# Optimization experiments

Hardware: AMD Instinct MI355X
Metric: run time of the kernel (lower is better)

The kernel has to match this reference:

```python
import jax, jax.numpy as jnp
import numpy as np

G, N, F_IN, H, C = 128, 512, 128, 128, 10
LAMB = 1.0
NEG_SLOPE = 0.2
P_EDGE = 32.0 / N  # avg degree ~32


def setup_inputs() -> dict:
    key = jax.random.key(0)
    ks = jax.random.split(key, 12)
    x = jax.random.normal(ks[0], (G, N, F_IN), dtype=jnp.float32)
    # symmetric 0/1 adjacency without self loops (per-graph dense block)
    a = (jax.random.uniform(ks[1], (G, N, N)) < P_EDGE).astype(jnp.float32)
    adj = jnp.maximum(a, jnp.swapaxes(a, 1, 2)) * (1.0 - jnp.eye(N, dtype=jnp.float32))

    def lin(k, fi, fo):
        return (jax.random.normal(k, (fi, fo), dtype=jnp.float32) / np.float32(np.sqrt(fi)))

    return {
        "x": x, "adj": adj,
        "W1": lin(ks[2], F_IN, H), "b1": jnp.zeros((H,), jnp.float32),
        "W2": lin(ks[3], H, H), "b2": jnp.zeros((H,), jnp.float32),
        "W3": lin(ks[4], H, H), "b3": jnp.zeros((H,), jnp.float32),
        "att1_s": 0.1 * jax.random.normal(ks[5], (H,), dtype=jnp.float32),
        "att1_d": 0.1 * jax.random.normal(ks[6], (H,), dtype=jnp.float32),
        "att2_s": 0.1 * jax.random.normal(ks[7], (H,), dtype=jnp.float32),
        "att2_d": 0.1 * jax.random.normal(ks[8], (H,), dtype=jnp.float32),
        "Wl1": lin(ks[9], 2 * H, H), "bl1": jnp.zeros((H,), jnp.float32),
        "Wl2": lin(ks[10], H, H // 2), "bl2": jnp.zeros((H // 2,), jnp.float32),
        "Wl3": lin(ks[11], H // 2, C), "bl3": jnp.zeros((C,), jnp.float32),
    }


def gcn(x, adj, W, b):
    # GCNConv: D^{-1/2} (A + I) D^{-1/2} X W + b  (self-loop weight 1, edge weights in adj)
    deg = adj.sum(-1) + 1.0                              # [G, n]
    dinv = jax.lax.rsqrt(deg)
    xw = x @ W                                           # [G, n, H]
    agg = jnp.einsum('gij,gjf->gif', adj, dinv[..., None] * xw)
    return dinv[..., None] * agg + (dinv * dinv)[..., None] * xw + b


def info_score(x, adj):
    # HGP-SL node information score: row-wise L1 norm of (I - D^{-1} A) X
    deg = jnp.maximum(adj.sum(-1), 1.0)
    agg = jnp.einsum('gij,gjf->gif', adj, x) / deg[..., None]
    return jnp.sum(jnp.abs(x - agg), axis=-1)            # [G, n]


def hgpsl_pool(x, adj, att_s, att_d, k):
    # top-k node selection by information score, then structure learning:
    # dense (sample=False) path: e_ij = leaky_relu(att.[x_i||x_j]) + lamb*A_ij, softmax over j
    s = info_score(x, adj)
    _, idx = jax.lax.top_k(s, k)                         # [G, k]
    xk = jnp.take_along_axis(x, idx[..., None], axis=1)  # [G, k, H]
    g = jnp.arange(x.shape[0])[:, None, None]
    ak = adj[g, idx[:, :, None], idx[:, None, :]]        # induced adjacency [G, k, k]
    e = jax.nn.leaky_relu((xk @ att_s)[:, :, None] + (xk @ att_d)[:, None, :], NEG_SLOPE)
    attn = jax.nn.softmax(e + LAMB * ak, axis=-1)        # new learned edge weights
    return xk, attn


def readout(x):
    # gmp || gap over nodes
    return jnp.concatenate([x.max(axis=1), x.mean(axis=1)], axis=-1)


def reference(x, adj, W1, b1, W2, b2, W3, b3, att1_s, att1_d, att2_s, att2_d,
              Wl1, bl1, Wl2, bl2, Wl3, bl3):
    h = jax.nn.relu(gcn(x, adj, W1, b1))
    h, a1 = hgpsl_pool(h, adj, att1_s, att1_d, N // 2)
    x1 = readout(h)
    h = jax.nn.relu(gcn(h, a1, W2, b2))
    h, a2 = hgpsl_pool(h, a1, att2_s, att2_d, N // 4)
    x2 = readout(h)
    h = jax.nn.relu(gcn(h, a2, W3, b3))
    x3 = readout(h)
    z = jax.nn.relu(x1) + jax.nn.relu(x2) + jax.nn.relu(x3)
    z = jax.nn.relu(z @ Wl1 + bl1)
    z = jax.nn.relu(z @ Wl2 + bl2)
    return jax.nn.softmax(z @ Wl3 + bl3, axis=-1)
```

## Files before the change

### kernel.cpp

```cpp
#include <hip/hip_runtime.h>

#define Gg   128
#define N1   512
#define FH   128
#define K1   256
#define K2   128

typedef __bf16 bf16x8 __attribute__((ext_vector_type(8)));
typedef float  floatx4 __attribute__((ext_vector_type(4)));

__device__ inline float wredsum(float v) {
#pragma unroll
    for (int o = 32; o; o >>= 1) v += __shfl_xor(v, o, 64);
    return v;
}
__device__ inline float wredmax(float v) {
#pragma unroll
    for (int o = 32; o; o >>= 1) v = fmaxf(v, __shfl_xor(v, o, 64));
    return v;
}
__device__ inline unsigned short bf_rne(float x) {
    unsigned u = __float_as_uint(x);
    return (unsigned short)((u + 0x7fffu + ((u >> 16) & 1u)) >> 16);
}
__device__ __forceinline__ void gll16(const void* gsrc, void* lds) {
    __builtin_amdgcn_global_load_lds(
        (const __attribute__((address_space(1))) unsigned int*)gsrc,
        (__attribute__((address_space(3))) unsigned int*)lds, 16, 0, 0);
}

__global__ __launch_bounds__(256) void k_prep(const float* __restrict__ adj,
        unsigned short* __restrict__ adjbf,
        float* __restrict__ dinv_gcn, float* __restrict__ dinv_info) {
    int wave = threadIdx.x >> 6, lane = threadIdx.x & 63;
    long long row = (long long)blockIdx.x * 4 + wave;
    const float* ar = adj + row * N1;
    float s = 0.f;
    unsigned short ub[8] __attribute__((aligned(16)));
#pragma unroll
    for (int c = 0; c < 2; ++c) {
        float4 v = *(const float4*)(ar + lane * 8 + c * 4);
        s += (v.x + v.y) + (v.z + v.w);
        ub[c * 4 + 0] = (unsigned short)(__float_as_uint(v.x) >> 16);
        ub[c * 4 + 1] = (unsigned short)(__float_as_uint(v.y) >> 16);
        ub[c * 4 + 2] = (unsigned short)(__float_as_uint(v.z) >> 16);
        ub[c * 4 + 3] = (unsigned short)(__float_as_uint(v.w) >> 16);
    }
    *(uint4*)(adjbf + row * N1 + lane * 8) = *(const uint4*)ub;
    s = wredsum(s);
    if (lane == 0) {
        dinv_gcn[row]  = rsqrtf(s + 1.0f);
        dinv_info[row] = 1.0f / fmaxf(s, 1.0f);
    }
}

__global__ __launch_bounds__(256) void k_tsplit(const float* __restrict__ feat,
        unsigned short* __restrict__ Thi, unsigned short* __restrict__ Tmid,
        unsigned short* __restrict__ Tlo) {
    __shared__ float tile[64 * 65];
    int b = blockIdx.x;
    int g = b >> 4, rb = (b >> 1) & 7, cb = b & 1;
    int t = threadIdx.x;
    {
        int r0 = t >> 4, c4 = t & 15;
#pragma unroll
        for (int i = 0; i < 4; ++i) {
            int r = r0 + i * 16;
            float4 v = *(const float4*)(feat + ((long long)g * 512 + rb * 64 + r) * 128 + cb * 64 + c4 * 4);
            tile[r * 65 + c4 * 4 + 0] = v.x;
            tile[r * 65 + c4 * 4 + 1] = v.y;
            tile[r * 65 + c4 * 4 + 2] = v.z;
            tile[r * 65 + c4 * 4 + 3] = v.w;
        }
    }
    __syncthreads();
    int tf = t >> 2, chunk = t & 3;
    unsigned short hbuf[16] __attribute__((aligned(16)));
    unsigned short mbuf[16] __attribute__((aligned(16)));
    unsigned short lbuf[16] __attribute__((aligned(16)));
#pragma unroll
    for (int i = 0; i < 16; ++i) {
        int m = chunk * 16 + i;
        float v = tile[m * 65 + tf];
        unsigned short h = bf_rne(v);
        float fh = __uint_as_float((unsigned)h << 16);
        float r1 = v - fh;
        unsigned short md = bf_rne(r1);
        float fm = __uint_as_float((unsigned)md << 16);
        float r2 = r1 - fm;
        unsigned short lo = bf_rne(r2);
        hbuf[i] = h; mbuf[i] = md; lbuf[i] = lo;
    }
    int sxz = (tf >> 1) & 3;
    int c0 = (chunk & 1) * 2;
    int p0 = (c0 ^ sxz) * 8, p1 = ((c0 + 1) ^ sxz) * 8;
    long long obase = (long long)g * 65536 + (rb * 2 + (chunk >> 1)) * 4096
                    + (cb * 64 + tf) * 32;
    *(uint4*)(Thi + obase + p0)  = *(const uint4*)&hbuf[0];
    *(uint4*)(Thi + obase + p1)  = *(const uint4*)&hbuf[8];
    *(uint4*)(Tmid + obase + p0) = *(const uint4*)&mbuf[0];
    *(uint4*)(Tmid + obase + p1) = *(const uint4*)&mbuf[8];
    *(uint4*)(Tlo + obase + p0)  = *(const uint4*)&lbuf[0];
    *(uint4*)(Tlo + obase + p1)  = *(const uint4*)&lbuf[8];
}

template<int EPI>
__global__ __launch_bounds__(256) void k_aggmm(const unsigned short* __restrict__ adjbf,
        const unsigned short* __restrict__ Bhi, const unsigned short* __restrict__ Bmid,
        const unsigned short* __restrict__ Blo,
        const float* __restrict__ dvec, const float* __restrict__ hx,
        const float* __restrict__ bias, float* __restrict__ outH, float* __restrict__ outS) {
    __shared__ unsigned short Al[4096];
    __shared__ unsigned short Blin[3][4096];
    __shared__ float sred[2][128];
    int b = blockIdx.x;
    int g  = (b & 7) + ((b >> 5) << 3);
    int rb = (b >> 3) & 3;
    int tid = threadIdx.x;
    int w = tid >> 6, lane = tid & 63;
    int wm = w >> 1, wn = w & 1;
    int ln = lane & 15, quad = lane >> 4;
    int aoff = ((quad ^ ((lane >> 1) & 3)) << 4);
    floatx4 acc[4][4];
#pragma unroll
    for (int i = 0; i < 4; ++i)
#pragma unroll
        for (int j = 0; j < 4; ++j) { floatx4 z = {0.f, 0.f, 0.f, 0.f}; acc[i][j] = z; }

    const char* bsrc0 = (const char*)(Bhi  + (long long)g * 65536);
    const char* bsrc1 = (const char*)(Bmid + (long long)g * 65536);
    const char* bsrc2 = (const char*)(Blo  + (long long)g * 65536);
    int r1 = w * 32 + (lane >> 2);
    int c1 = (lane & 3) ^ ((r1 >> 1) & 3);
    int r2 = r1 + 16;
    int c2 = (lane & 3) ^ ((r2 >> 1) & 3);
    const unsigned short* abase = adjbf + ((long long)g * 512 + rb * 128) * 512;
    const unsigned short* asrc1 = abase + (long long)r1 * 512 + c1 * 8;
    const unsigned short* asrc2 = abase + (long long)r2 * 512 + c2 * 8;
    char* aldst = (char*)Al + w * 2048;

    for (int kk = 0; kk < 512; kk += 32) {
        __syncthreads();
        gll16(asrc1 + kk, aldst);
        gll16(asrc2 + kk, aldst + 1024);
        {
            long long soff = (long long)(kk >> 5) * 8192 + (w * 2048) + (lane << 4);
            char* l0 = (char*)&Blin[0][0] + w * 2048;
            char* l1 = (char*)&Blin[1][0] + w * 2048;
            char* l2 = (char*)&Blin[2][0] + w * 2048;
            gll16(bsrc0 + soff,        l0);
            gll16(bsrc0 + soff + 1024, l0 + 1024);
            gll16(bsrc1 + soff,        l1);
            gll16(bsrc1 + soff + 1024, l1 + 1024);
            gll16(bsrc2 + soff,        l2);
            gll16(bsrc2 + soff + 1024, l2 + 1024);
        }
        __syncthreads();
        bf16x8 af[4];
#pragma unroll
        for (int tm = 0; tm < 4; ++tm)
            af[tm] = *(const bf16x8*)((const char*)Al + (wm * 64 + tm * 16 + ln) * 64 + aoff);
#pragma unroll
        for (int s = 0; s < 3; ++s) {
#pragma unroll
            for (int tn = 0; tn < 4; ++tn) {
                bf16x8 bfr = *(const bf16x8*)((const char*)&Blin[s][0]
                                              + (wn * 64 + tn * 16 + ln) * 64 + aoff);
#pragma unroll
                for (int tm = 0; tm < 4; ++tm)
                    acc[tm][tn] = __builtin_amdgcn_mfma_f32_16x16x32_bf16(af[tm], bfr, acc[tm][tn], 0, 0, 0);
            }
        }
    }
    long long rowbase = (long long)g * 512 + rb * 128;
    if (EPI == 0) {
#pragma unroll
        for (int tm = 0; tm < 4; ++tm)
#pragma unroll
        for (int r = 0; r < 4; ++r) {
            int ml = wm * 64 + tm * 16 + quad * 4 + r;
            long long grow = rowbase + ml;
            float di = dvec[grow];
#pragma unroll
            for (int tn = 0; tn < 4; ++tn) {
                int nc = wn * 64 + tn * 16 + ln;
                float hv = hx[grow * 128 + nc];
                float o = fmaxf(fmaf(di, acc[tm][tn][r] + hv, bias[nc]), 0.f);
                outH[grow * 128 + nc] = o;
            }
        }
    } else {
#pragma unroll
        for (int tm = 0; tm < 4; ++tm)
#pragma unroll
        for (int r = 0; r < 4; ++r) {
            int ml = wm * 64 + tm * 16 + quad * 4 + r;
            long long grow = rowbase + ml;
            float di = dvec[grow];
            float v = 0.f;
#pragma unroll
            for (int tn = 0; tn < 4; ++tn) {
                int nc = wn * 64 + tn * 16 + ln;
                float hv = hx[grow * 128 + nc];
                v += fabsf(hv - acc[tm][tn][r] * di);
            }
            v += __shfl_xor(v, 1); v += __shfl_xor(v, 2);
            v += __shfl_xor(v, 4); v += __shfl_xor(v, 8);
            if (ln == 0) sred[wn][ml] = v;
        }
        __syncthreads();
        if (tid < 128) outS[rowbase + tid] = sred[0][tid] + sred[1][tid];
    }
}

__global__ __launch_bounds__(256) void k_gemm_rw(const float* __restrict__ A,
        const float* __restrict__ W, float* __restrict__ C,
        const float* __restrict__ rs) {
    __shared__ float Al[64][68];
    __shared__ float Wl[64][132];
    long long row0 = (long long)blockIdx.x * 64;
    int tid = threadIdx.x, tr = tid >> 4, tc = tid & 15;
    float acc[4][8] = {};
    for (int ch = 0; ch < 2; ++ch) {
        for (int p = tid; p < 1024; p += 256) {
            int r = p >> 4, c4 = p & 15;
            *(float4*)&Al[r][c4 * 4] = *(const float4*)(A + (row0 + r) * 128 + ch * 64 + c4 * 4);
        }
        for (int p = tid; p < 2048; p += 256) {
            int r = p >> 5, c4 = p & 31;
            *(float4*)&Wl[r][c4 * 4] = *(const float4*)(W + (ch * 64 + r) * 128 + c4 * 4);
        }
        __syncthreads();
        for (int k = 0; k < 64; ++k) {
            float4 w0 = *(const float4*)&Wl[k][tc * 8];
            float4 w1 = *(const float4*)&Wl[k][tc * 8 + 4];
            float w[8] = {w0.x, w0.y, w0.z, w0.w, w1.x, w1.y, w1.z, w1.w};
#pragma unroll
            for (int i = 0; i < 4; ++i) {
                float a = Al[tr * 4 + i][k];
#pragma unroll
                for (int j = 0; j < 8; ++j) acc[i][j] = fmaf(a, w[j], acc[i][j]);
            }
        }
        __syncthreads();
    }
#pragma unroll
    for (int i = 0; i < 4; ++i) {
        long long r = row0 + tr * 4 + i;
        float sc = rs ? rs[r] : 1.0f;
        *(float4*)(C + r * 128 + tc * 8)     = make_float4(sc * acc[i][0], sc * acc[i][1], sc * acc[i][2], sc * acc[i][3]);
        *(float4*)(C + r * 128 + tc * 8 + 4) = make_float4(sc * acc[i][4], sc * acc[i][5], sc * acc[i][6], sc * acc[i][7]);
    }
}

template<int NT, int KSEL>
__global__ __launch_bounds__(256) void k_topk(const float* __restrict__ s, int* __restrict__ idx) {
    __shared__ unsigned long long keys[NT];
    int g = blockIdx.x;
    const float* sg = s + g * NT;
    for (int t = threadIdx.x; t < NT; t += 256) {
        unsigned int b = __float_as_uint(sg[t]);
        unsigned int ord = (b & 0x80000000u) ? ~b : (b | 0x80000000u);
        keys[t] = ((unsigned long long)(~ord) << 32) | (unsigned int)t;
    }
    __syncthreads();
    for (int k = 2; k <= NT; k <<= 1) {
        for (int j = k >> 1; j > 0; j >>= 1) {
            for (int i = threadIdx.x; i < NT; i += 256) {
                int l = i ^ j;
                if (l > i) {
                    bool dir = ((i & k) == 0);
                    unsigned long long a = keys[i], b2 = keys[l];
                    bool sw = dir ? (a > b2) : (a < b2);
                    if (sw) { keys[i] = b2; keys[l] = a; }
                }
            }
            __syncthreads();
        }
    }
    for (int t = threadIdx.x; t < KSEL; t += 256)
        idx[g * KSEL + t] = (int)(keys[t] & 0xffffffffu);
}

template<int KK>
__global__ __launch_bounds__(256) void k_gather(const float* __restrict__ h, int srcN,
        const int* __restrict__ idx, const float* __restrict__ atts, const float* __restrict__ attd,
        float* __restrict__ xk, float* __restrict__ as_, float* __restrict__ ad_) {
    int wave = threadIdx.x >> 6, lane = threadIdx.x & 63;
    int r = blockIdx.x * 4 + wave;
    int g = r / KK;
    int j = idx[r];
    float2 v = *(const float2*)(h + ((long long)g * srcN + j) * 128 + lane * 2);
    *(float2*)(xk + (long long)r * 128 + lane * 2) = v;
    float2 sv = *(const float2*)(atts + lane * 2);
    float2 dv = *(const float2*)(attd + lane * 2);
    float ps = v.x * sv.x + v.y * sv.y;
    float pd = v.x * dv.x + v.y * dv.y;
    ps = wredsum(ps); pd = wredsum(pd);
    if (lane == 0) { as_[r] = ps; ad_[r] = pd; }
}

template<int KK, int SRCN>
__global__ __launch_bounds__(256) void k_attn(const float* __restrict__ adjSrc,
        const int* __restrict__ idx, const float* __restrict__ as_, const float* __restrict__ ad_,
        float* __restrict__ attn, float* __restrict__ dgo, float* __restrict__ dio) {
    constexpr int E = KK / 64;
    __shared__ int   idxL[KK];
    __shared__ float adL[KK];
    __shared__ float rowL[4][SRCN];
    int bpg = KK / 4;
    int g = blockIdx.x / bpg;
    int wave = threadIdx.x >> 6, lane = threadIdx.x & 63;
    int i = (blockIdx.x % bpg) * 4 + wave;
    for (int t = threadIdx.x; t < KK; t += 256) { idxL[t] = idx[g * KK + t]; adL[t] = ad_[g * KK + t]; }
    __syncthreads();
    int ri = idxL[i];
    const float* arow = adjSrc + ((long long)g * SRCN + ri) * SRCN;
    for (int c = lane; c < SRCN; c += 64) rowL[wave][c] = arow[c];
    float asi = as_[g * KK + i];
    float vals[E];
    float m = -1e30f;
#pragma unroll
    for (int e = 0; e < E; ++e) {
        int j = e * 64 + lane;
        float x = asi + adL[j];
        x = (x >= 0.f) ? x : 0.2f * x;
        x += rowL[wave][idxL[j]];
        vals[e] = x; m = fmaxf(m, x);
    }
    m = wredmax(m);
    float S = 0.f;
#pragma unroll
    for (int e = 0; e < E; ++e) { vals[e] = expf(vals[e] - m); S += vals[e]; }
    S = wredsum(S);
    float inv = 1.f / S, rs = 0.f;
    float* orow = attn + ((long long)g * KK + i) * KK;
#pragma unroll
    for (int e = 0; e < E; ++e) { float p = vals[e] * inv; rs += p; orow[e * 64 + lane] = p; }
    rs = wredsum(rs);
    if (lane == 0) { dgo[g * KK + i] = rsqrtf(rs + 1.f); dio[g * KK + i] = 1.f / fmaxf(rs, 1.f); }
}

template<int KK>
__global__ __launch_bounds__(128) void k_readout(const float* __restrict__ xk, float* __restrict__ xo) {
    int g = blockIdx.x, f = threadIdx.x;
    const float* p = xk + (long long)g * KK * 128 + f;
    float m = -1e30f, s = 0.f;
    for (int r = 0; r < KK; ++r) { float v = p[r * 128]; m = fmaxf(m, v); s += v; }
    xo[g * 256 + f] = m;
    xo[g * 256 + 128 + f] = s * (1.0f / KK);
}

template<int KK, bool SCALEY, int EPI>
__global__ __launch_bounds__(256) void k_agg(const float* __restrict__ A, const float* __restrict__ Y,
        const float* __restrict__ dg, const float* __restrict__ di_,
        const float* __restrict__ bias, const float* __restrict__ hx,
        float* __restrict__ outH, float* __restrict__ outS) {
    __shared__ float Al[64][68];
    __shared__ float Yl[64][132];
    __shared__ float red[64][17];
    constexpr int RB = KK / 64;
    int g = blockIdx.x / RB;
    int rb = blockIdx.x % RB;
    const float* Ag = A + (long long)g * KK * KK;
    const float* Yg = Y + (long long)g * KK * 128;
    int tid = threadIdx.x, tr = tid >> 4, tc = tid & 15;
    float acc[4][8] = {};
    for (int ch = 0; ch < KK / 64; ++ch) {
        for (int p = tid; p < 1024; p += 256) {
            int r = p >> 4, c4 = p & 15;
            *(float4*)&Al[r][c4 * 4] = *(const float4*)(Ag + (rb * 64 + r) * KK + ch * 64 + c4 * 4);
        }
        for (int p = tid; p < 2048; p += 256) {
            int r = p >> 5, c4 = p & 31;
            float4 v = *(const float4*)(Yg + (ch * 64 + r) * 128 + c4 * 4);
            if (SCALEY) { float sc = dg[g * KK + ch * 64 + r]; v.x *= sc; v.y *= sc; v.z *= sc; v.w *= sc; }
            *(float4*)&Yl[r][c4 * 4] = v;
        }
        __syncthreads();
        for (int k = 0; k < 64; ++k) {
            float4 w0 = *(const float4*)&Yl[k][tc * 8];
            float4 w1 = *(const float4*)&Yl[k][tc * 8 + 4];
            float w[8] = {w0.x, w0.y, w0.z, w0.w, w1.x, w1.y, w1.z, w1.w};
#pragma unroll
            for (int i = 0; i < 4; ++i) {
                float a = Al[tr * 4 + i][k];
#pragma unroll
                for (int j = 0; j < 8; ++j) acc[i][j] = fmaf(a, w[j], acc[i][j]);
            }
        }
        __syncthreads();
    }
    int i0 = rb * 64 + tr * 4;
    if (EPI == 0) {
#pragma unroll
        for (int i = 0; i < 4; ++i) {
            long long gi = (long long)g * KK + i0 + i;
            float d = dg[gi], dd = d * d;
            float4 x0 = *(const float4*)(hx + gi * 128 + tc * 8);
            float4 x1 = *(const float4*)(hx + gi * 128 + tc * 8 + 4);
            float4 b0 = *(const float4*)(bias + tc * 8);
            float4 b1 = *(const float4*)(bias + tc * 8 + 4);
            float4 o0, o1;
            o0.x = fmaxf(fmaf(d, acc[i][0], fmaf(dd, x0.x, b0.x)), 0.f);
            o0.y = fmaxf(fmaf(d, acc[i][1], fmaf(dd, x0.y, b0.y)), 0.f);
            o0.z = fmaxf(fmaf(d, acc[i][2], fmaf(dd, x0.z, b0.z)), 0.f);
            o0.w = fmaxf(fmaf(d, acc[i][3], fmaf(dd, x0.w, b0.w)), 0.f);
            o1.x = fmaxf(fmaf(d, acc[i][4], fmaf(dd, x1.x, b1.x)), 0.f);
            o1.y = fmaxf(fmaf(d, acc[i][5], fmaf(dd, x1.y, b1.y)), 0.f);
            o1.z = fmaxf(fmaf(d, acc[i][6], fmaf(dd, x1.z, b1.z)), 0.f);
            o1.w = fmaxf(fmaf(d, acc[i][7], fmaf(dd, x1.w, b1.w)), 0.f);
            *(float4*)(outH + gi * 128 + tc * 8)     = o0;
            *(float4*)(outH + gi * 128 + tc * 8 + 4) = o1;
        }
    } else {
#pragma unroll
        for (int i = 0; i < 4; ++i) {
            long long gi = (long long)g * KK + i0 + i;
            float d = di_[gi];
            float4 x0 = *(const float4*)(hx + gi * 128 + tc * 8);
            float4 x1 = *(const float4*)(hx + gi * 128 + tc * 8 + 4);
            float p = fabsf(x0.x - acc[i][0] * d) + fabsf(x0.y - acc[i][1] * d)
                    + fabsf(x0.z - acc[i][2] * d) + fabsf(x0.w - acc[i][3] * d)
                    + fabsf(x1.x - acc[i][4] * d) + fabsf(x1.y - acc[i][5] * d)
                    + fabsf(x1.z - acc[i][6] * d) + fabsf(x1.w - acc[i][7] * d);
            red[tr * 4 + i][tc] = p;
        }
        __syncthreads();
        if (tid < 64) {
            float s = 0.f;
#pragma unroll
            for (int t = 0; t < 16; ++t) s += red[tid][t];
            outS[(long long)g * KK + rb * 64 + tid] = s;
        }
    }
}

__global__ __launch_bounds__(128) void k_mlp(const float* __restrict__ x1, const float* __restrict__ x2,
        const float* __restrict__ x3,
        const float* __restrict__ Wl1, const float* __restrict__ bl1,
        const float* __restrict__ Wl2, const float* __restrict__ bl2,
        const float* __restrict__ Wl3, const float* __restrict__ bl3,
        float* __restrict__ out) {
    __shared__ float z[256], z1[128], z2[64], lg[10];
    int g = blockIdx.x, t = threadIdx.x;
    for (int k = t; k < 256; k += 128)
        z[k] = fmaxf(x1[g * 256 + k], 0.f) + fmaxf(x2[g * 256 + k], 0.f) + fmaxf(x3[g * 256 + k], 0.f);
    __syncthreads();
    {
        float acc = bl1[t];
        for (int k = 0; k < 256; ++k) acc = fmaf(z[k], Wl1[k * 128 + t], acc);
        z1[t] = fmaxf(acc, 0.f);
    }
    __syncthreads();
    if (t < 64) {
        float acc = bl2[t];
        for (int k = 0; k < 128; ++k) acc = fmaf(z1[k], Wl2[k * 64 + t], acc);
        z2[t] = fmaxf(acc, 0.f);
    }
    __syncthreads();
    if (t < 10) {
        float acc = bl3[t];
        for (int k = 0; k < 64; ++k) acc = fmaf(z2[k], Wl3[k * 10 + t], acc);
        lg[t] = acc;
    }
    __syncthreads();
    if (t == 0) {
        float m = -1e30f;
        for (int c = 0; c < 10; ++c) m = fmaxf(m, lg[c]);
        float S = 0.f;
        float e[10];
        for (int c = 0; c < 10; ++c) { e[c] = expf(lg[c] - m); S += e[c]; }
        float inv = 1.f / S;
        for (int c = 0; c < 10; ++c) out[g * 10 + c] = e[c] * inv;
    }
}

extern "C" void kernel_launch(void* const* d_in, const int* in_sizes, int n_in,
                              void* d_out, int out_size, void* d_ws, size_t ws_size,
                              hipStream_t stream) {
    const float* x     = (const float*)d_in[0];
    const float* adj   = (const float*)d_in[1];
    const float* W1    = (const float*)d_in[2];
    const float* b1    = (const float*)d_in[3];
    const float* W2    = (const float*)d_in[4];
    const float* b2    = (const float*)d_in[5];
    const float* W3    = (const float*)d_in[6];
    const float* b3    = (const float*)d_in[7];
    const float* att1s = (const float*)d_in[8];
    const float* att1d = (const float*)d_in[9];
    const float* att2s = (const float*)d_in[10];
    const float* att2d = (const float*)d_in[11];
    const float* Wl1   = (const float*)d_in[12];
    const float* bl1   = (const float*)d_in[13];
    const float* Wl2   = (const float*)d_in[14];
    const float* bl2   = (const float*)d_in[15];
    const float* Wl3   = (const float*)d_in[16];
    const float* bl3   = (const float*)d_in[17];
    float* out = (float*)d_out;

    char* ws = (char*)d_ws;
    unsigned short* Thi  = (unsigned short*)(ws + 0);
    unsigned short* Tmid = (unsigned short*)(ws + 16777216);
    unsigned short* Tlo  = (unsigned short*)(ws + 33554432);
    float* xk1 = (float*)(ws + 0);
    float* xw2 = (float*)(ws + 16777216);
    float* h2  = (float*)(ws + 33554432);
    float* xk2 = (float*)(ws + 16777216);
    float* a2  = (float*)(ws + 25165824);
    float* xw3 = (float*)(ws + 0);
    float* h3  = (float*)(ws + 8388608);
    float* dxw1 = (float*)(ws + 50331648);
    float* h1   = dxw1;
    float* a1   = dxw1;
    float* s1      = (float*)(ws + 83886080);
    int*   idx1    = (int*)  (ws + 84148224);
    float* as1     = (float*)(ws + 84279296);
    float* ad1     = (float*)(ws + 84410368);
    float* dinv_g1 = (float*)(ws + 84541440);
    float* dinv_i1 = (float*)(ws + 84803584);
    float* dinv_g2 = (float*)(ws + 85065728);
    float* dinv_i2 = (float*)(ws + 85196800);
    float* x1r     = (float*)(ws + 85327872);
    float* s2      = (float*)(ws + 85458944);
    int*   idx2    = (int*)  (ws + 85590016);
    float* as2     = (float*)(ws + 85655552);
    float* ad2     = (float*)(ws + 85721088);
    float* dinv_g3 = (float*)(ws + 85786624);
    float* dinv_i3 = (float*)(ws + 85852160);
    float* x2r     = (float*)(ws + 85917696);
    float* x3r     = (float*)(ws + 86048768);
    unsigned short* adjbf = (unsigned short*)(ws + 100663296);

    k_prep<<<Gg * N1 / 4, 256, 0, stream>>>(adj, adjbf, dinv_g1, dinv_i1);
    k_gemm_rw<<<Gg * N1 / 64, 256, 0, stream>>>(x, W1, dxw1, dinv_g1);
    k_tsplit<<<Gg * 16, 256, 0, stream>>>(dxw1, Thi, Tmid, Tlo);
    k_aggmm<0><<<Gg * 4, 256, 0, stream>>>(adjbf, Thi, Tmid, Tlo, dinv_g1, dxw1, b1, h1, nullptr);
    k_tsplit<<<Gg * 16, 256, 0, stream>>>(h1, Thi, Tmid, Tlo);
    k_aggmm<1><<<Gg * 4, 256, 0, stream>>>(adjbf, Thi, Tmid, Tlo, dinv_i1, h1, nullptr, nullptr, s1);
    k_topk<N1, K1><<<Gg, 256, 0, stream>>>(s1, idx1);
    k_gather<K1><<<Gg * K1 / 4, 256, 0, stream>>>(h1, N1, idx1, att1s, att1d, xk1, as1, ad1);
    k_readout<K1><<<Gg, 128, 0, stream>>>(xk1, x1r);
    k_attn<K1, N1><<<Gg * K1 / 4, 256, 0, stream>>>(adj, idx1, as1, ad1, a1, dinv_g2, dinv_i2);

    k_gemm_rw<<<Gg * K1 / 64, 256, 0, stream>>>(xk1, W2, xw2, nullptr);
    k_agg<K1, true, 0><<<Gg * (K1 / 64), 256, 0, stream>>>(a1, xw2, dinv_g2, dinv_i2, b2, xw2, h2, nullptr);
    k_agg<K1, false, 1><<<Gg * (K1 / 64), 256, 0, stream>>>(a1, h2, dinv_g2, dinv_i2, b2, h2, nullptr, s2);
    k_topk<K1, K2><<<Gg, 256, 0, stream>>>(s2, idx2);
    k_gather<K2><<<Gg * K2 / 4, 256, 0, stream>>>(h2, K1, idx2, att2s, att2d, xk2, as2, ad2);
    k_readout<K2><<<Gg, 128, 0, stream>>>(xk2, x2r);
    k_attn<K2, K1><<<Gg * K2 / 4, 256, 0, stream>>>(a1, idx2, as2, ad2, a2, dinv_g3, dinv_i3);

    k_gemm_rw<<<Gg * K2 / 64, 256, 0, stream>>>(xk2, W3, xw3, nullptr);
    k_agg<K2, true, 0><<<Gg * (K2 / 64), 256, 0, stream>>>(a2, xw3, dinv_g3, dinv_i3, b3, xw3, h3, nullptr);
    k_readout<K2><<<Gg, 128, 0, stream>>>(h3, x3r);

    k_mlp<<<Gg, 128, 0, stream>>>(x1r, x2r, x3r, Wl1, bl1, Wl2, bl2, Wl3, bl3, out);
}
```

Measured before the change: 607.6 us.

## Double-buffer LDS tiles in aggregation GEMM to overlap loads with MFMA

Adds a second LDS buffer for the adjacency and three-way split B tiles in k_aggmm, so the global-to-LDS loads for the next K step are issued before the MFMAs on the current step. Partial vmcnt waits and raw s_barrier calls take the place of the two __syncthreads per iteration. The aim is to hide global load latency behind matrix math. In exchange, LDS use per block roughly doubles, which may lower occupancy, and correctness now depends on the hand-written waitcnt count matching the eight outstanding loads.

```diff
diff --git a/kernel.cpp b/kernel.cpp
--- a/kernel.cpp
+++ b/kernel.cpp
@@ -110,8 +110,8 @@
         const unsigned short* __restrict__ Blo,
         const float* __restrict__ dvec, const float* __restrict__ hx,
         const float* __restrict__ bias, float* __restrict__ outH, float* __restrict__ outS) {
-    __shared__ unsigned short Al[4096];
-    __shared__ unsigned short Blin[3][4096];
+    __shared__ unsigned short Al[2][4096];
+    __shared__ unsigned short Blin[2][3][4096];
     __shared__ float sred[2][128];
     int b = blockIdx.x;
     int g  = (b & 7) + ((b >> 5) << 3);
@@ -137,41 +137,53 @@
     const unsigned short* abase = adjbf + ((long long)g * 512 + rb * 128) * 512;
     const unsigned short* asrc1 = abase + (long long)r1 * 512 + c1 * 8;
     const unsigned short* asrc2 = abase + (long long)r2 * 512 + c2 * 8;
-    char* aldst = (char*)Al + w * 2048;
-
+
+#define STAGE(bi, kkv) do {                                                   \
+        char* aldst = (char*)&Al[bi][0] + w * 2048;                           \
+        gll16(asrc1 + (kkv), aldst);                                          \
+        gll16(asrc2 + (kkv), aldst + 1024);                                   \
+        long long soff = (long long)((kkv) >> 5) * 8192 + (w * 2048) + (lane << 4); \
+        char* l0 = (char*)&Blin[bi][0][0] + w * 2048;                         \
+        char* l1 = (char*)&Blin[bi][1][0] + w * 2048;                         \
+        char* l2 = (char*)&Blin[bi][2][0] + w * 2048;                         \
+        gll16(bsrc0 + soff,        l0);                                       \
+        gll16(bsrc0 + soff + 1024, l0 + 1024);                                \
+        gll16(bsrc1 + soff,        l1);                                       \
+        gll16(bsrc1 + soff + 1024, l1 + 1024);                                \
+        gll16(bsrc2 + soff,        l2);                                       \
+        gll16(bsrc2 + soff + 1024, l2 + 1024);                                \
+    } while (0)
+
+    STAGE(0, 0);
     for (int kk = 0; kk < 512; kk += 32) {
-        __syncthreads();
-        gll16(asrc1 + kk, aldst);
-        gll16(asrc2 + kk, aldst + 1024);
-        {
-            long long soff = (long long)(kk >> 5) * 8192 + (w * 2048) + (lane << 4);
-            char* l0 = (char*)&Blin[0][0] + w * 2048;
-            char* l1 = (char*)&Blin[1][0] + w * 2048;
-            char* l2 = (char*)&Blin[2][0] + w * 2048;
-            gll16(bsrc0 + soff,        l0);
-            gll16(bsrc0 + soff + 1024, l0 + 1024);
-            gll16(bsrc1 + soff,        l1);
-            gll16(bsrc1 + soff + 1024, l1 + 1024);
-            gll16(bsrc2 + soff,        l2);
-            gll16(bsrc2 + soff + 1024, l2 + 1024);
-        }
-        __syncthreads();
+        int cur = (kk >> 5) & 1;
+        if (kk + 32 < 512) {
+            STAGE(cur ^ 1, kk + 32);
+            asm volatile("s_waitcnt vmcnt(8)" ::: "memory");
+        } else {
+            asm volatile("s_waitcnt vmcnt(0)" ::: "memory");
+        }
+        __builtin_amdgcn_sched_barrier(0);
+        __builtin_amdgcn_s_barrier();
         bf16x8 af[4];
 #pragma unroll
         for (int tm = 0; tm < 4; ++tm)
-            af[tm] = *(const bf16x8*)((const char*)Al + (wm * 64 + tm * 16 + ln) * 64 + aoff);
+            af[tm] = *(const bf16x8*)((const char*)&Al[cur][0] + (wm * 64 + tm * 16 + ln) * 64 + aoff);
 #pragma unroll
         for (int s = 0; s < 3; ++s) {
 #pragma unroll
             for (int tn = 0; tn < 4; ++tn) {
-                bf16x8 bfr = *(const bf16x8*)((const char*)&Blin[s][0]
+                bf16x8 bfr = *(const bf16x8*)((const char*)&Blin[cur][s][0]
                                               + (wn * 64 + tn * 16 + ln) * 64 + aoff);
 #pragma unroll
                 for (int tm = 0; tm < 4; ++tm)
                     acc[tm][tn] = __builtin_amdgcn_mfma_f32_16x16x32_bf16(af[tm], bfr, acc[tm][tn], 0, 0, 0);
             }
         }
-    }
+        __builtin_amdgcn_sched_barrier(0);
+        __builtin_amdgcn_s_barrier();
+    }
+#undef STAGE
     long long rowbase = (long long)g * 512 + rb * 128;
     if (EPI == 0) {
 #pragma unroll
```

Result: no change. 608.3 us (+0.1%).
